# Kernel tuning notes

Hardware: AMD Instinct MI355X
Metric: run time of the kernel (lower is better)

## Reference

```python
import jax, jax.numpy as jnp
import numpy as np

N, C, H, W = 8, 32, 224, 224
TM = 4


def setup_inputs() -> dict:
    key = jax.random.key(0)
    k1, k2 = jax.random.split(key)
    inputs = jax.random.normal(k1, (N, C, H, W), dtype=jnp.float32)
    # learned per-(tm, channel) perspective params: identity + small perturbation
    ident = jnp.array([1, 0, 0, 0, 1, 0, 0, 0], dtype=jnp.float32)
    wt_pers = ident[None, None, :] + 0.05 * jax.random.normal(k2, (TM, C, 8), dtype=jnp.float32)
    return {"inputs": inputs, "wt_pers": wt_pers}


def _perspective_forward(inputs, wt_pers):
    # inputs: (N, C, H, W); wt_pers: (TM, C, 8)
    n, ch, h, w = inputs.shape
    tm = wt_pers.shape[0]
    dt = inputs.dtype

    # get_theta_matrix: append trailing identity param (eye(3).flatten()[8:] == [1.0])
    theta = jnp.concatenate([wt_pers, jnp.ones((tm, ch, 1), dt)], axis=-1)
    pers = theta.reshape(tm, ch, 3, 3)

    # generate_grids: torch.meshgrid(x(len W), y(len H), indexing='ij') -> (W, H), flatten,
    # matmul, then view as (3, H, W). Replicate exactly (flatten of (W,H) reshaped to (H,W)).
    xs = jnp.linspace(-1.0, 1.0, w).astype(dt)
    ys = jnp.linspace(-1.0, 1.0, h).astype(dt)
    xg, yg = jnp.meshgrid(xs, ys, indexing='ij')  # (W, H)
    grid = jnp.stack([xg.ravel(), yg.ravel(), jnp.ones(w * h, dt)], axis=0)  # (3, W*H)

    bg = jnp.einsum('tcij,jp->tcip', pers, grid).reshape(tm, ch, 3, h, w)
    omega = bg[:, :, 2]
    x_s = bg[:, :, 0] / omega
    y_s = bg[:, :, 1] / omega

    # interpolate (faithful, incl. the (max-1) scaling and the wb weight as written)
    max_x = float(w - 1)
    max_y = float(h - 1)
    x = 0.5 * ((x_s + 1.0) * (max_x - 1.0))
    y = 0.5 * ((y_s + 1.0) * (max_y - 1.0))
    x0 = jnp.floor(x).astype(jnp.int32)
    x1 = x0 + 1
    y0 = jnp.floor(y).astype(jnp.int32)
    y1 = y0 + 1
    x0 = jnp.clip(x0, 0, w - 1)
    x1 = jnp.clip(x1, 0, w - 1)
    y0 = jnp.clip(y0, 0, h - 1)
    y1 = jnp.clip(y1, 0, h - 1)

    cidx = jnp.arange(ch).reshape(1, ch, 1, 1)

    def gather(yy, xx):
        # fancy index: (N basic) x (tm,ch,H,W advanced) -> (N, tm, ch, H, W)
        return inputs[:, cidx, yy, xx]

    Ia = gather(y0, x0)
    Ib = gather(y1, x0)
    Ic = gather(y0, x1)
    Id = gather(y1, x1)

    x0f = x0.astype(dt); x1f = x1.astype(dt)
    y0f = y0.astype(dt); y1f = y1.astype(dt)
    wa = (x1f - x) * (y1f - y)
    wb = (x1f - x) * (y1f - y0f)  # source uses (y1 - y0) here, not (y - y0)
    wc = (x - x0f) * (y1f - y)
    wd = (x - x0f) * (y - y0f)

    out = wa * Ia + wb * Ib + wc * Ic + wd * Id  # (N, tm, ch, H, W)
    # original: cat over tm at dim -1 -> (N,C,H,W,tm); permute(0,1,4,2,3); flatten(1,2)
    return out.transpose(0, 2, 1, 3, 4).reshape(n, ch * tm, h, w)


def reference(inputs, wt_pers):
    return _perspective_forward(inputs, wt_pers)
```

## Files before the change

### kernel.cpp

```cpp
#include <hip/hip_runtime.h>

#define N_  8
#define C_  32
#define H_  224
#define W_  224
#define TM_ 4
#define TA  32
#define TB  32

__global__ __launch_bounds__(256) void persp_kernel(
    const float* __restrict__ inp,
    const float* __restrict__ wt,
    float* __restrict__ out)
{
    __shared__ float tile[N_][TA][TB + 1];

    const int tid = threadIdx.x;
    const int c   = blockIdx.y;
    const int ta  = blockIdx.x / (W_ / TB);
    const int tb  = blockIdx.x % (W_ / TB);
    const int a0  = ta * TA;
    const int b0  = tb * TB;

    const int a_off = tid & 31;
    const int bgrp  = tid >> 5;
    const int a     = a0 + a_off;

    const float step = 2.0f / 223.0f;
    const float hx   = -1.0f + (float)a * step;

    const int j  = tid & 31;
    const int i0 = tid >> 5;

    const size_t plane   = (size_t)H_ * W_;
    const size_t istride = (size_t)C_ * plane;
    const size_t ostride = (size_t)(C_ * TM_) * plane;

    for (int t = 0; t < TM_; ++t) {
        const float* th = wt + ((size_t)t * C_ + c) * 8;
        const float t0 = th[0], t1 = th[1], t2 = th[2], t3 = th[3];
        const float t4 = th[4], t5 = th[5], t6 = th[6], t7 = th[7];

        int   iA[4], iB[4], iC[4], iD[4];
        float wa[4], wb[4], wc[4], wd[4];

#pragma unroll
        for (int p = 0; p < 4; ++p) {
            const int b = b0 + bgrp + 8 * p;
            const float hy = -1.0f + (float)b * step;

            const float w0 = t0 * hx + t1 * hy + t2;
            const float w1 = t3 * hx + t4 * hy + t5;
            const float w2 = t6 * hx + t7 * hy + 1.0f;

            const float xs = w0 / w2;
            const float ys = w1 / w2;

            const float x = 0.5f * ((xs + 1.0f) * 222.0f);
            const float y = 0.5f * ((ys + 1.0f) * 222.0f);

            int x0i = (int)floorf(x);
            int y0i = (int)floorf(y);
            int x1i = x0i + 1;
            int y1i = y0i + 1;
            x0i = min(max(x0i, 0), W_ - 1);
            x1i = min(max(x1i, 0), W_ - 1);
            y0i = min(max(y0i, 0), H_ - 1);
            y1i = min(max(y1i, 0), H_ - 1);

            const float x0f = (float)x0i, x1f = (float)x1i;
            const float y0f = (float)y0i, y1f = (float)y1i;

            wa[p] = (x1f - x) * (y1f - y);
            wb[p] = (x1f - x) * (y1f - y0f);
            wc[p] = (x - x0f) * (y1f - y);
            wd[p] = (x - x0f) * (y - y0f);

            iA[p] = y0i * W_ + x0i;
            iB[p] = y1i * W_ + x0i;
            iC[p] = y0i * W_ + x1i;
            iD[p] = y1i * W_ + x1i;
        }

#pragma unroll
        for (int n = 0; n < N_; ++n) {
            const float* ib = inp + (size_t)n * istride + (size_t)c * plane;
#pragma unroll
            for (int p = 0; p < 4; ++p) {
                const float Ia = ib[iA[p]];
                const float Ib = ib[iB[p]];
                const float Ic = ib[iC[p]];
                const float Id = ib[iD[p]];
                tile[n][a_off][bgrp + 8 * p] =
                    wa[p] * Ia + wb[p] * Ib + wc[p] * Ic + wd[p] * Id;
            }
        }
        __syncthreads();

        float* ob = out + ((size_t)(c * TM_ + t)) * plane + (size_t)a0 * W_ + b0;
#pragma unroll
        for (int n = 0; n < N_; ++n) {
            float* obn = ob + (size_t)n * ostride;
#pragma unroll
            for (int k = 0; k < 4; ++k) {
                const int i = i0 + 8 * k;
                obn[(size_t)i * W_ + j] = tile[n][i][j];
            }
        }
        __syncthreads();
    }
}

extern "C" void kernel_launch(void* const* d_in, const int* in_sizes, int n_in,
                              void* d_out, int out_size, void* d_ws, size_t ws_size,
                              hipStream_t stream) {
    const float* inp = (const float*)d_in[0];
    const float* wt  = (const float*)d_in[1];
    float* out = (float*)d_out;

    dim3 grid((H_ / TA) * (W_ / TB), C_);
    persp_kernel<<<grid, 256, 0, stream>>>(inp, wt, out);
}
```

Measured before the change: 343.3 us.

## Halve shared tile, process batch in two chunks, use float4 stores

```diff
diff --git a/kernel.cpp b/kernel.cpp
--- a/kernel.cpp
+++ b/kernel.cpp
@@ -7,13 +7,14 @@
 #define TM_ 4
 #define TA  32
 #define TB  32
+#define NC  4
 
-__global__ __launch_bounds__(256) void persp_kernel(
+__global__ __launch_bounds__(256, 8) void persp_kernel(
     const float* __restrict__ inp,
     const float* __restrict__ wt,
     float* __restrict__ out)
 {
-    __shared__ float tile[N_][TA][TB + 1];
+    __shared__ float tile[NC][TA][TB + 1];
 
     const int tid = threadIdx.x;
     const int c   = blockIdx.y;
@@ -29,12 +30,14 @@
     const float step = 2.0f / 223.0f;
     const float hx   = -1.0f + (float)a * step;
 
-    const int j  = tid & 31;
-    const int i0 = tid >> 5;
+    const int j4 = (tid & 7) * 4;
+    const int iw = tid >> 3;
 
     const size_t plane   = (size_t)H_ * W_;
     const size_t istride = (size_t)C_ * plane;
     const size_t ostride = (size_t)(C_ * TM_) * plane;
+
+    const float* ibase = inp + (size_t)c * plane;
 
     for (int t = 0; t < TM_; ++t) {
         const float* th = wt + ((size_t)t * C_ + c) * 8;
@@ -83,31 +86,38 @@
         }
 
 #pragma unroll
-        for (int n = 0; n < N_; ++n) {
-            const float* ib = inp + (size_t)n * istride + (size_t)c * plane;
+        for (int nh = 0; nh < N_ / NC; ++nh) {
 #pragma unroll
-            for (int p = 0; p < 4; ++p) {
-                const float Ia = ib[iA[p]];
-                const float Ib = ib[iB[p]];
-                const float Ic = ib[iC[p]];
-                const float Id = ib[iD[p]];
-                tile[n][a_off][bgrp + 8 * p] =
-                    wa[p] * Ia + wb[p] * Ib + wc[p] * Ic + wd[p] * Id;
+            for (int nn = 0; nn < NC; ++nn) {
+                const int n = nh * NC + nn;
+                const float* ib = ibase + (size_t)n * istride;
+#pragma unroll
+                for (int p = 0; p < 4; ++p) {
+                    const float Ia = ib[iA[p]];
+                    const float Ib = ib[iB[p]];
+                    const float Ic = ib[iC[p]];
+                    const float Id = ib[iD[p]];
+                    tile[nn][a_off][bgrp + 8 * p] =
+                        wa[p] * Ia + wb[p] * Ib + wc[p] * Ic + wd[p] * Id;
+                }
             }
+            __syncthreads();
+
+#pragma unroll
+            for (int nn = 0; nn < NC; ++nn) {
+                const int n = nh * NC + nn;
+                float4 v;
+                v.x = tile[nn][iw][j4 + 0];
+                v.y = tile[nn][iw][j4 + 1];
+                v.z = tile[nn][iw][j4 + 2];
+                v.w = tile[nn][iw][j4 + 3];
+                float* op = out + (size_t)n * ostride
+                                + ((size_t)(c * TM_ + t)) * plane
+                                + (size_t)(a0 + iw) * W_ + (b0 + j4);
+                *reinterpret_cast<float4*>(op) = v;
+            }
+            __syncthreads();
         }
-        __syncthreads();
-
-        float* ob = out + ((size_t)(c * TM_ + t)) * plane + (size_t)a0 * W_ + b0;
-#pragma unroll
-        for (int n = 0; n < N_; ++n) {
-            float* obn = ob + (size_t)n * ostride;
-#pragma unroll
-            for (int k = 0; k < 4; ++k) {
-                const int i = i0 + 8 * k;
-                obn[(size_t)i * W_ + j] = tile[n][i][j];
-            }
-        }
-        __syncthreads();
     }
 }
 
```

New measurement: 333.1 us. 3.0% less time.

## Reorder loops over batch outer, recompute coords, vectorize nontemporal output stores

Applied to the files above, without the earlier changes.

```diff
diff --git a/kernel.cpp b/kernel.cpp
--- a/kernel.cpp
+++ b/kernel.cpp
@@ -8,12 +8,14 @@
 #define TA  32
 #define TB  32
 
-__global__ __launch_bounds__(256) void persp_kernel(
+typedef float fx4 __attribute__((ext_vector_type(4)));
+
+__global__ __launch_bounds__(256, 8) void persp_kernel(
     const float* __restrict__ inp,
     const float* __restrict__ wt,
     float* __restrict__ out)
 {
-    __shared__ float tile[N_][TA][TB + 1];
+    __shared__ float tile[TM_][TA][TB + 1];
 
     const int tid = threadIdx.x;
     const int c   = blockIdx.y;
@@ -29,83 +31,87 @@
     const float step = 2.0f / 223.0f;
     const float hx   = -1.0f + (float)a * step;
 
-    const int j  = tid & 31;
-    const int i0 = tid >> 5;
+    const int j4 = (tid & 7) * 4;
+    const int iw = tid >> 3;
 
     const size_t plane   = (size_t)H_ * W_;
     const size_t istride = (size_t)C_ * plane;
     const size_t ostride = (size_t)(C_ * TM_) * plane;
 
-    for (int t = 0; t < TM_; ++t) {
-        const float* th = wt + ((size_t)t * C_ + c) * 8;
-        const float t0 = th[0], t1 = th[1], t2 = th[2], t3 = th[3];
-        const float t4 = th[4], t5 = th[5], t6 = th[6], t7 = th[7];
+    float th[TM_][8];
+#pragma unroll
+    for (int t = 0; t < TM_; ++t)
+#pragma unroll
+        for (int k = 0; k < 8; ++k)
+            th[t][k] = wt[((size_t)t * C_ + c) * 8 + k];
 
-        int   iA[4], iB[4], iC[4], iD[4];
-        float wa[4], wb[4], wc[4], wd[4];
+    const float* ibase = inp + (size_t)c * plane;
+    float* obase = out + ((size_t)c * TM_) * plane + (size_t)(a0 + iw) * W_ + (b0 + j4);
+
+    for (int n = 0; n < N_; ++n) {
+        const float* ib = ibase + (size_t)n * istride;
 
 #pragma unroll
-        for (int p = 0; p < 4; ++p) {
-            const int b = b0 + bgrp + 8 * p;
-            const float hy = -1.0f + (float)b * step;
-
-            const float w0 = t0 * hx + t1 * hy + t2;
-            const float w1 = t3 * hx + t4 * hy + t5;
-            const float w2 = t6 * hx + t7 * hy + 1.0f;
-
-            const float xs = w0 / w2;
-            const float ys = w1 / w2;
-
-            const float x = 0.5f * ((xs + 1.0f) * 222.0f);
-            const float y = 0.5f * ((ys + 1.0f) * 222.0f);
-
-            int x0i = (int)floorf(x);
-            int y0i = (int)floorf(y);
-            int x1i = x0i + 1;
-            int y1i = y0i + 1;
-            x0i = min(max(x0i, 0), W_ - 1);
-            x1i = min(max(x1i, 0), W_ - 1);
-            y0i = min(max(y0i, 0), H_ - 1);
-            y1i = min(max(y1i, 0), H_ - 1);
-
-            const float x0f = (float)x0i, x1f = (float)x1i;
-            const float y0f = (float)y0i, y1f = (float)y1i;
-
-            wa[p] = (x1f - x) * (y1f - y);
-            wb[p] = (x1f - x) * (y1f - y0f);
-            wc[p] = (x - x0f) * (y1f - y);
-            wd[p] = (x - x0f) * (y - y0f);
-
-            iA[p] = y0i * W_ + x0i;
-            iB[p] = y1i * W_ + x0i;
-            iC[p] = y0i * W_ + x1i;
-            iD[p] = y1i * W_ + x1i;
-        }
-
-#pragma unroll
-        for (int n = 0; n < N_; ++n) {
-            const float* ib = inp + (size_t)n * istride + (size_t)c * plane;
+        for (int t = 0; t < TM_; ++t) {
 #pragma unroll
             for (int p = 0; p < 4; ++p) {
-                const float Ia = ib[iA[p]];
-                const float Ib = ib[iB[p]];
-                const float Ic = ib[iC[p]];
-                const float Id = ib[iD[p]];
-                tile[n][a_off][bgrp + 8 * p] =
-                    wa[p] * Ia + wb[p] * Ib + wc[p] * Ic + wd[p] * Id;
+                const int b = b0 + bgrp + 8 * p;
+                const float hy = -1.0f + (float)b * step;
+
+                const float w0 = th[t][0] * hx + th[t][1] * hy + th[t][2];
+                const float w1 = th[t][3] * hx + th[t][4] * hy + th[t][5];
+                const float w2 = th[t][6] * hx + th[t][7] * hy + 1.0f;
+
+                const float rw = 1.0f / w2;
+                const float xs = w0 * rw;
+                const float ys = w1 * rw;
+
+                const float x = 0.5f * ((xs + 1.0f) * 222.0f);
+                const float y = 0.5f * ((ys + 1.0f) * 222.0f);
+
+                int x0i = (int)floorf(x);
+                int y0i = (int)floorf(y);
+                int x1i = x0i + 1;
+                int y1i = y0i + 1;
+                x0i = min(max(x0i, 0), W_ - 1);
+                x1i = min(max(x1i, 0), W_ - 1);
+                y0i = min(max(y0i, 0), H_ - 1);
+                y1i = min(max(y1i, 0), H_ - 1);
+
+                const float x0f = (float)x0i, x1f = (float)x1i;
+                const float y0f = (float)y0i, y1f = (float)y1i;
+
+                const float wa = (x1f - x) * (y1f - y);
+                const float wb = (x1f - x) * (y1f - y0f);
+                const float wc = (x - x0f) * (y1f - y);
+                const float wd = (x - x0f) * (y - y0f);
+
+                const int iA = y0i * W_ + x0i;
+                const int iB = y1i * W_ + x0i;
+                const int iC = y0i * W_ + x1i;
+                const int iD = y1i * W_ + x1i;
+
+                const float Ia = ib[iA];
+                const float Ib = ib[iB];
+                const float Ic = ib[iC];
+                const float Id = ib[iD];
+
+                tile[t][a_off][bgrp + 8 * p] =
+                    wa * Ia + wb * Ib + wc * Ic + wd * Id;
             }
         }
         __syncthreads();
 
-        float* ob = out + ((size_t)(c * TM_ + t)) * plane + (size_t)a0 * W_ + b0;
+        float* on = obase + (size_t)n * ostride;
 #pragma unroll
-        for (int n = 0; n < N_; ++n) {
-            float* obn = ob + (size_t)n * ostride;
-#pragma unroll
-            for (int k = 0; k < 4; ++k) {
-                const int i = i0 + 8 * k;
-                obn[(size_t)i * W_ + j] = tile[n][i][j];
-            }
+        for (int t = 0; t < TM_; ++t) {
+            fx4 v;
+            v.x = tile[t][iw][j4 + 0];
+            v.y = tile[t][iw][j4 + 1];
+            v.z = tile[t][iw][j4 + 2];
+            v.w = tile[t][iw][j4 + 3];
+            __builtin_nontemporal_store(
+                v, reinterpret_cast<fx4*>(on + (size_t)t * plane));
         }
         __syncthreads();
     }
```

Result: slower. 731.0 us (+112.9%).

## Assign one wavefront per tm, drop block barriers, prefetch next batch gathers

Applied to the files above, without the earlier changes.

```diff
diff --git a/kernel.cpp b/kernel.cpp
--- a/kernel.cpp
+++ b/kernel.cpp
@@ -5,48 +5,49 @@
 #define H_  224
 #define W_  224
 #define TM_ 4
-#define TA  32
-#define TB  32
 
-__global__ __launch_bounds__(256) void persp_kernel(
+__global__ __launch_bounds__(256, 4) void persp_kernel(
     const float* __restrict__ inp,
     const float* __restrict__ wt,
     float* __restrict__ out)
 {
-    __shared__ float tile[N_][TA][TB + 1];
+    __shared__ float lds[TM_][2][32][17];
 
-    const int tid = threadIdx.x;
-    const int c   = blockIdx.y;
-    const int ta  = blockIdx.x / (W_ / TB);
-    const int tb  = blockIdx.x % (W_ / TB);
-    const int a0  = ta * TA;
-    const int b0  = tb * TB;
+    const int tid   = threadIdx.x;
+    const int t     = tid >> 6;
+    const int lane  = tid & 63;
+    const int a_off = lane & 31;
+    const int half  = lane >> 5;
 
-    const int a_off = tid & 31;
-    const int bgrp  = tid >> 5;
-    const int a     = a0 + a_off;
+    const int c  = blockIdx.y;
+    const int ta = blockIdx.x / 7;
+    const int tb = blockIdx.x % 7;
+    const int a0 = ta * 32;
+    const int b0 = tb * 32;
 
     const float step = 2.0f / 223.0f;
-    const float hx   = -1.0f + (float)a * step;
+    const float hx   = -1.0f + (float)(a0 + a_off) * step;
 
-    const int j  = tid & 31;
-    const int i0 = tid >> 5;
+    const int rrow = lane >> 2;
+    const int rcol = (lane & 3) * 4;
 
     const size_t plane   = (size_t)H_ * W_;
     const size_t istride = (size_t)C_ * plane;
     const size_t ostride = (size_t)(C_ * TM_) * plane;
 
-    for (int t = 0; t < TM_; ++t) {
-        const float* th = wt + ((size_t)t * C_ + c) * 8;
-        const float t0 = th[0], t1 = th[1], t2 = th[2], t3 = th[3];
-        const float t4 = th[4], t5 = th[5], t6 = th[6], t7 = th[7];
+    const float* th = wt + ((size_t)t * C_ + c) * 8;
+    const float t0 = th[0], t1 = th[1], t2 = th[2], t3 = th[3];
+    const float t4 = th[4], t5 = th[5], t6 = th[6], t7 = th[7];
 
-        int   iA[4], iB[4], iC[4], iD[4];
-        float wa[4], wb[4], wc[4], wd[4];
+    const float* ibc = inp + (size_t)c * plane;
+    float* oc = out + (size_t)(c * TM_ + t) * plane;
 
+    for (int ph = 0; ph < 2; ++ph) {
+        int   iA[8], iB[8], dx[8];
+        float wa_[8], wb_[8], wc_[8], wd_[8];
 #pragma unroll
-        for (int p = 0; p < 4; ++p) {
-            const int b = b0 + bgrp + 8 * p;
+        for (int p = 0; p < 8; ++p) {
+            const int b = b0 + half + 2 * (ph * 8 + p);
             const float hy = -1.0f + (float)b * step;
 
             const float w0 = t0 * hx + t1 * hy + t2;
@@ -71,43 +72,59 @@
             const float x0f = (float)x0i, x1f = (float)x1i;
             const float y0f = (float)y0i, y1f = (float)y1i;
 
-            wa[p] = (x1f - x) * (y1f - y);
-            wb[p] = (x1f - x) * (y1f - y0f);
-            wc[p] = (x - x0f) * (y1f - y);
-            wd[p] = (x - x0f) * (y - y0f);
+            wa_[p] = (x1f - x) * (y1f - y);
+            wb_[p] = (x1f - x) * (y1f - y0f);
+            wc_[p] = (x - x0f) * (y1f - y);
+            wd_[p] = (x - x0f) * (y - y0f);
 
             iA[p] = y0i * W_ + x0i;
             iB[p] = y1i * W_ + x0i;
-            iC[p] = y0i * W_ + x1i;
-            iD[p] = y1i * W_ + x1i;
+            dx[p] = x1i - x0i;
+        }
+
+        float gA[8], gB[8], gC[8], gD[8];
+#pragma unroll
+        for (int p = 0; p < 8; ++p) {
+            gA[p] = ibc[iA[p]];
+            gC[p] = ibc[iA[p] + dx[p]];
+            gB[p] = ibc[iB[p]];
+            gD[p] = ibc[iB[p] + dx[p]];
         }
 
 #pragma unroll
         for (int n = 0; n < N_; ++n) {
-            const float* ib = inp + (size_t)n * istride + (size_t)c * plane;
 #pragma unroll
-            for (int p = 0; p < 4; ++p) {
-                const float Ia = ib[iA[p]];
-                const float Ib = ib[iB[p]];
-                const float Ic = ib[iC[p]];
-                const float Id = ib[iD[p]];
-                tile[n][a_off][bgrp + 8 * p] =
-                    wa[p] * Ia + wb[p] * Ib + wc[p] * Ic + wd[p] * Id;
+            for (int p = 0; p < 8; ++p)
+                lds[t][n & 1][a_off][half + 2 * p] =
+                    wa_[p] * gA[p] + wb_[p] * gB[p] +
+                    wc_[p] * gC[p] + wd_[p] * gD[p];
+
+            if (n < N_ - 1) {
+                const float* ib = ibc + (size_t)(n + 1) * istride;
+#pragma unroll
+                for (int p = 0; p < 8; ++p) {
+                    gA[p] = ib[iA[p]];
+                    gC[p] = ib[iA[p] + dx[p]];
+                    gB[p] = ib[iB[p]];
+                    gD[p] = ib[iB[p] + dx[p]];
+                }
+            }
+
+            asm volatile("s_waitcnt lgkmcnt(0)" ::: "memory");
+
+            float* on = oc + (size_t)n * ostride + (size_t)a0 * W_
+                           + (b0 + 16 * ph);
+#pragma unroll
+            for (int k = 0; k < 2; ++k) {
+                const int i = rrow + 16 * k;
+                float4 v;
+                v.x = lds[t][n & 1][i][rcol + 0];
+                v.y = lds[t][n & 1][i][rcol + 1];
+                v.z = lds[t][n & 1][i][rcol + 2];
+                v.w = lds[t][n & 1][i][rcol + 3];
+                *reinterpret_cast<float4*>(on + (size_t)i * W_ + rcol) = v;
             }
         }
-        __syncthreads();
-
-        float* ob = out + ((size_t)(c * TM_ + t)) * plane + (size_t)a0 * W_ + b0;
-#pragma unroll
-        for (int n = 0; n < N_; ++n) {
-            float* obn = ob + (size_t)n * ostride;
-#pragma unroll
-            for (int k = 0; k < 4; ++k) {
-                const int i = i0 + 8 * k;
-                obn[(size_t)i * W_ + j] = tile[n][i][j];
-            }
-        }
-        __syncthreads();
     }
 }
 
@@ -118,6 +135,6 @@
     const float* wt  = (const float*)d_in[1];
     float* out = (float*)d_out;
 
-    dim3 grid((H_ / TA) * (W_ / TB), C_);
+    dim3 grid(7 * 7, C_);
     persp_kernel<<<grid, 256, 0, stream>>>(inp, wt, out);
 }
```

Result: slower. 498.7 us (+45.3%).
